# Kernel optimization log

Hardware: AMD Instinct MI355X
Metric: run time of the kernel (lower is better)

The kernel has to match this reference:

```python
import jax, jax.numpy as jnp
import numpy as np

N = 100000   # num nodes
E = 1600000  # num edges (avg degree 16)
D = 32       # input_dim == latent_size
L = 3        # num_layers
K = 3        # num_hops


def setup_inputs() -> dict:
    key = jax.random.key(0)
    k0, k1, k2, k3, k4 = jax.random.split(key, 5)
    x = jax.random.normal(k0, (N, D), dtype=jnp.float32)
    edge_index = jax.random.randint(k1, (2, E), 0, N, dtype=jnp.int32)
    edge_weight = jax.random.uniform(k2, (E,), dtype=jnp.float32)
    # TAGConv per layer: K+1 bias-free Linear(in,out) weights + one bias
    W = jax.random.normal(k3, (L, K + 1, D, D), dtype=jnp.float32) * (1.0 / np.sqrt(D))
    b = jax.random.normal(k4, (L, D), dtype=jnp.float32) * 0.01
    return {"x": x, "edge_index": edge_index, "edge_weight": edge_weight, "W": W, "b": b}


def reference(x, edge_index, edge_weight, W, b):
    row, col = edge_index[0], edge_index[1]  # source, target
    # PyG gcn_norm with add_self_loops=False: deg at target, symmetric norm
    deg = jax.ops.segment_sum(edge_weight, col, num_segments=N)
    safe = jnp.where(deg > 0, deg, 1.0)
    dis = jnp.where(deg > 0, jax.lax.rsqrt(safe), 0.0)  # deg^{-1/2}
    norm = dis[row] * edge_weight * dis[col]            # [E]
    for l in range(L):
        out = x @ W[l, 0]
        h = x
        for k in range(1, K + 1):
            # one hop of normalized sparse aggregation: out[col] += norm * h[row]
            h = jax.ops.segment_sum(h[row] * norm[:, None], col, num_segments=N)
            out = out + h @ W[l, k]
        x = jax.nn.relu(out + b[l])
    return x
```

## Files before the change

### kernel.cpp

```cpp
#include <hip/hip_runtime.h>
#include <hip/hip_fp16.h>

#define NN 100000
#define NE 1600000
#define DD 32
#define NL 3
#define NK 3

#define BK 512
#define NBK ((NN + BK - 1) / BK)
#define EA 4096
#define GA ((NE + EA - 1) / EA)
#define NCNT (NBK * GA)
#define NSC ((NCNT + 255) / 256)
#define CB (NN * DD / 4 / 256)

typedef _Float16 half8 __attribute__((ext_vector_type(8)));
typedef float f32x4 __attribute__((ext_vector_type(4)));

__global__ void countA_kernel(const int* __restrict__ col, unsigned* __restrict__ cntAB,
                              const float* __restrict__ x, __half* __restrict__ xh,
                              const float* __restrict__ W, half8* __restrict__ Bpk) {
    __shared__ unsigned hc[NBK];
    int bid = blockIdx.x;
    int t = threadIdx.x;
    if (bid < GA) {
        for (int i = t; i < NBK; i += 256) hc[i] = 0;
        __syncthreads();
        int e0 = bid * EA;
        int e1 = e0 + EA; if (e1 > NE) e1 = NE;
        for (int e = e0 + t; e < e1; e += 256)
            atomicAdd(&hc[((unsigned)col[e]) >> 9], 1u);
        __syncthreads();
        for (int i = t; i < NBK; i += 256)
            cntAB[i * GA + bid] = hc[i];
    } else if (bid < GA + CB) {
        int i = (bid - GA) * 256 + t;
        f32x4 v = ((const f32x4*)x)[i];
        __half2 h01 = __floats2half2_rn(v.x, v.y);
        __half2 h23 = __floats2half2_rn(v.z, v.w);
        int2 o;
        o.x = *(int*)&h01; o.y = *(int*)&h23;
        ((int2*)xh)[i] = o;
    } else if (t < 64) {
        int l = bid - GA - CB;
        int m = t & 15, kq = t >> 4;
        for (int c = 0; c < 4; ++c) {
            for (int h = 0; h < 2; ++h) {
                half8 hi, lo;
                for (int j = 0; j < 8; ++j) {
                    float wv = W[(size_t)((l * 4 + c) * DD + kq * 8 + j) * DD + h * 16 + m];
                    _Float16 wh = (_Float16)wv;
                    hi[j] = wh;
                    lo[j] = (_Float16)(wv - (float)wh);
                }
                Bpk[(size_t)(((l * 4 + c) * 2 + h) * 2 + 0) * 64 + t] = hi;
                Bpk[(size_t)(((l * 4 + c) * 2 + h) * 2 + 1) * 64 + t] = lo;
            }
        }
    }
}

__global__ void scanb_kernel(unsigned* __restrict__ a, unsigned* __restrict__ bsum) {
    __shared__ unsigned s[256];
    int t = threadIdx.x;
    int i = blockIdx.x * 256 + t;
    unsigned v = (i < NCNT) ? a[i] : 0u;
    s[t] = v;
    __syncthreads();
    for (int off = 1; off < 256; off <<= 1) {
        unsigned add = (t >= off) ? s[t - off] : 0u;
        __syncthreads();
        s[t] += add;
        __syncthreads();
    }
    if (i < NCNT) a[i] = s[t] - v;
    if (t == 255) bsum[blockIdx.x] = s[255];
}

__global__ void scant_kernel(unsigned* __restrict__ bsum) {
    __shared__ unsigned s[512];
    int t = threadIdx.x;
    unsigned v = (t < NSC) ? bsum[t] : 0u;
    s[t] = v;
    __syncthreads();
    for (int off = 1; off < 512; off <<= 1) {
        unsigned add = (t >= off) ? s[t - off] : 0u;
        __syncthreads();
        s[t] += add;
        __syncthreads();
    }
    if (t < NSC) bsum[t] = s[t] - v;
}

__global__ void scana_kernel(unsigned* __restrict__ a, const unsigned* __restrict__ bsum,
                             unsigned* __restrict__ bbase) {
    int i = blockIdx.x * 256 + threadIdx.x;
    if (i < NCNT) {
        unsigned v = a[i] + bsum[i >> 8];
        a[i] = v;
        if (i % GA == 0) bbase[i / GA] = v;
    }
    if (i == 0) bbase[NBK] = NE;
}

__global__ void scatterC_kernel(const int* __restrict__ row, const int* __restrict__ col,
                                const float* __restrict__ w,
                                const unsigned* __restrict__ cntAB, int2* __restrict__ eb) {
    __shared__ unsigned cur[NBK];
    int bid = blockIdx.x;
    int t = threadIdx.x;
    for (int i = t; i < NBK; i += 256) cur[i] = cntAB[i * GA + bid];
    __syncthreads();
    int e0 = bid * EA;
    int e1 = e0 + EA; if (e1 > NE) e1 = NE;
    for (int e = e0 + t; e < e1; e += 256) {
        unsigned c = (unsigned)col[e];
        unsigned pos = atomicAdd(&cur[c >> 9], 1u);
        eb[pos] = make_int2((int)(((c & 511u) << 17) | (unsigned)row[e]),
                            __float_as_int(w[e]));
    }
}

__global__ void histD1_kernel(const int2* __restrict__ eb, const unsigned* __restrict__ bbase,
                              int* __restrict__ ptr, float* __restrict__ dis) {
    __shared__ unsigned h[BK];
    __shared__ unsigned ps[256];
    int b = blockIdx.x;
    int t = threadIdx.x;
    h[t] = 0; h[t + 256] = 0;
    __syncthreads();
    unsigned e0 = bbase[b], e1 = bbase[b + 1];
    for (unsigned e = e0 + t; e < e1; e += 256) {
        int2 E = eb[e];
        unsigned cl = ((unsigned)E.x) >> 17;
        float wv = __int_as_float(E.y);
        atomicAdd(&h[cl], (1u << 24) | (unsigned)(wv * 131072.0f));
    }
    __syncthreads();
    unsigned c0 = h[2 * t] >> 24, c1 = h[2 * t + 1] >> 24;
    unsigned pv = c0 + c1;
    ps[t] = pv;
    __syncthreads();
    for (int off = 1; off < 256; off <<= 1) {
        unsigned add = (t >= off) ? ps[t - off] : 0u;
        __syncthreads();
        ps[t] += add;
        __syncthreads();
    }
    unsigned base = e0 + ps[t] - pv;
    int n0 = b * BK + 2 * t;
    if (n0 < NN) {
        ptr[n0] = (int)base;
        float dg = (float)(h[2 * t] & 0xFFFFFFu) * (1.0f / 131072.0f);
        dis[n0] = dg > 0.f ? rsqrtf(dg) : 0.f;
    }
    if (n0 + 1 < NN) {
        ptr[n0 + 1] = (int)(base + c0);
        float dg = (float)(h[2 * t + 1] & 0xFFFFFFu) * (1.0f / 131072.0f);
        dis[n0 + 1] = dg > 0.f ? rsqrtf(dg) : 0.f;
    }
    if (b == 0 && t == 0) ptr[NN] = NE;
}

__global__ void fillD2_kernel(const int2* __restrict__ eb, const unsigned* __restrict__ bbase,
                              const int* __restrict__ ptr, const float* __restrict__ dis,
                              unsigned* __restrict__ epair) {
    __shared__ unsigned cur[BK];
    __shared__ float dl[BK];
    int b = blockIdx.x;
    int t = threadIdx.x;
    int n0 = b * BK;
    for (int i = t; i < BK; i += 256) {
        int n = n0 + i;
        cur[i] = (n < NN) ? (unsigned)ptr[n] : 0u;
        dl[i] = (n < NN) ? dis[n] : 0.f;
    }
    __syncthreads();
    unsigned e0 = bbase[b], e1 = bbase[b + 1];
    for (unsigned e = e0 + t; e < e1; e += 256) {
        int2 E = eb[e];
        unsigned cl = ((unsigned)E.x) >> 17;
        unsigned r = ((unsigned)E.x) & 0x1FFFFu;
        float nv = dis[r] * __int_as_float(E.y) * dl[cl];
        unsigned pos = atomicAdd(&cur[cl], 1u);
        unsigned hb = (unsigned)__half_as_ushort(__float2half(nv));
        epair[pos] = (hb << 17) | r;
    }
}

#define ACC8(rw, vv)                                                             \
    {                                                                            \
        float2 f0 = __half22float2(*reinterpret_cast<__half2*>(&rw.x));          \
        float2 f1 = __half22float2(*reinterpret_cast<__half2*>(&rw.y));          \
        float2 f2 = __half22float2(*reinterpret_cast<__half2*>(&rw.z));          \
        float2 f3 = __half22float2(*reinterpret_cast<__half2*>(&rw.w));          \
        agg[0] = fmaf(vv, f0.x, agg[0]); agg[1] = fmaf(vv, f0.y, agg[1]);        \
        agg[2] = fmaf(vv, f1.x, agg[2]); agg[3] = fmaf(vv, f1.y, agg[3]);        \
        agg[4] = fmaf(vv, f2.x, agg[4]); agg[5] = fmaf(vv, f2.y, agg[5]);        \
        agg[6] = fmaf(vv, f3.x, agg[6]); agg[7] = fmaf(vv, f3.y, agg[7]);        \
    }

__device__ __forceinline__ void gather_body16(const ushort* __restrict__ hin,
                                              const unsigned* __restrict__ epair,
                                              int p0, int p1, int st, int c4,
                                              float agg[8]) {
    const int4* hin4 = (const int4*)hin;
    for (int e = p0 + st; e < p1; e += 16) {
        int eA = e;
        int eB = (e + 4  < p1) ? e + 4  : p1 - 1;
        int eC = (e + 8  < p1) ? e + 8  : p1 - 1;
        int eD = (e + 12 < p1) ? e + 12 : p1 - 1;
        unsigned pA = epair[eA];
        unsigned pB = epair[eB];
        unsigned pC = epair[eC];
        unsigned pD = epair[eD];
        int4 rA = hin4[(size_t)(pA & 0x1FFFFu) * 4 + c4];
        int4 rB = hin4[(size_t)(pB & 0x1FFFFu) * 4 + c4];
        int4 rC = hin4[(size_t)(pC & 0x1FFFFu) * 4 + c4];
        int4 rD = hin4[(size_t)(pD & 0x1FFFFu) * 4 + c4];
        float vA = __half2float(__ushort_as_half((unsigned short)(pA >> 17)));
        float vB = (e + 4  < p1) ? __half2float(__ushort_as_half((unsigned short)(pB >> 17))) : 0.f;
        float vC = (e + 8  < p1) ? __half2float(__ushort_as_half((unsigned short)(pC >> 17))) : 0.f;
        float vD = (e + 12 < p1) ? __half2float(__ushort_as_half((unsigned short)(pD >> 17))) : 0.f;
        ACC8(rA, vA);
        ACC8(rB, vB);
        ACC8(rC, vC);
        ACC8(rD, vD);
    }
    #pragma unroll
    for (int i = 0; i < 8; ++i) {
        agg[i] += __shfl_xor(agg[i], 4, 16);
        agg[i] += __shfl_xor(agg[i], 8, 16);
    }
}

__global__ __launch_bounds__(256) void gather_kernel(
    const ushort* __restrict__ hin, ushort* __restrict__ hout,
    const int* __restrict__ ptr, const unsigned* __restrict__ epair) {
    int tid = threadIdx.x;
    int lane16 = tid & 15;
    int st = lane16 >> 2, c4 = lane16 & 3;
    int n = blockIdx.x * 16 + (tid >> 4);
    int p0 = ptr[n], p1 = ptr[n + 1];
    float agg[8] = {0.f, 0.f, 0.f, 0.f, 0.f, 0.f, 0.f, 0.f};
    gather_body16(hin, epair, p0, p1, st, c4, agg);
    if (lane16 < 4) {
        __half2 ha = __floats2half2_rn(agg[0], agg[1]);
        __half2 hb = __floats2half2_rn(agg[2], agg[3]);
        __half2 hc = __floats2half2_rn(agg[4], agg[5]);
        __half2 hd = __floats2half2_rn(agg[6], agg[7]);
        int4 pkv;
        pkv.x = *(int*)&ha; pkv.y = *(int*)&hb;
        pkv.z = *(int*)&hc; pkv.w = *(int*)&hd;
        ((int4*)hout)[(size_t)n * 4 + lane16] = pkv;
    }
}

__global__ __launch_bounds__(256) void k3ep_kernel(
    const ushort* __restrict__ f0, const ushort* __restrict__ h1,
    const ushort* __restrict__ h2,
    ushort* __restrict__ f0out, float* __restrict__ outf,
    const int* __restrict__ ptr, const unsigned* __restrict__ epair,
    const half8* __restrict__ Bp, const float* __restrict__ bias, int last) {
    __shared__ __half ldsH[16 * DD];
    int tid = threadIdx.x;
    int lane16 = tid & 15;
    int st = lane16 >> 2, c4 = lane16 & 3;
    int nloc = tid >> 4;
    int n0 = blockIdx.x * 16;
    int n = n0 + nloc;
    int p0 = ptr[n], p1 = ptr[n + 1];
    float agg[8] = {0.f, 0.f, 0.f, 0.f, 0.f, 0.f, 0.f, 0.f};
    gather_body16(h2, epair, p0, p1, st, c4, agg);
    if (lane16 < 4) {
        __half2 ha = __floats2half2_rn(agg[0], agg[1]);
        __half2 hb = __floats2half2_rn(agg[2], agg[3]);
        __half2 hc = __floats2half2_rn(agg[4], agg[5]);
        __half2 hd = __floats2half2_rn(agg[6], agg[7]);
        int4 pkv;
        pkv.x = *(int*)&ha; pkv.y = *(int*)&hb;
        pkv.z = *(int*)&hc; pkv.w = *(int*)&hd;
        *(int4*)&ldsH[nloc * DD + lane16 * 8] = pkv;
    }
    __syncthreads();
    if (tid < 64) {
        int m = tid & 15, kq = tid >> 4;
        int ai = (n0 + m) * 4 + kq;
        const half8* A0 = (const half8*)f0;
        const half8* A1 = (const half8*)h1;
        const half8* A2 = (const half8*)h2;
        f32x4 acc0 = {0.f, 0.f, 0.f, 0.f};
        f32x4 acc1 = {0.f, 0.f, 0.f, 0.f};
        half8 a;
        a = A0[ai];
        acc0 = __builtin_amdgcn_mfma_f32_16x16x32_f16(a, Bp[0 * 64 + tid], acc0, 0, 0, 0);
        acc0 = __builtin_amdgcn_mfma_f32_16x16x32_f16(a, Bp[1 * 64 + tid], acc0, 0, 0, 0);
        acc1 = __builtin_amdgcn_mfma_f32_16x16x32_f16(a, Bp[2 * 64 + tid], acc1, 0, 0, 0);
        acc1 = __builtin_amdgcn_mfma_f32_16x16x32_f16(a, Bp[3 * 64 + tid], acc1, 0, 0, 0);
        a = A1[ai];
        acc0 = __builtin_amdgcn_mfma_f32_16x16x32_f16(a, Bp[4 * 64 + tid], acc0, 0, 0, 0);
        acc0 = __builtin_amdgcn_mfma_f32_16x16x32_f16(a, Bp[5 * 64 + tid], acc0, 0, 0, 0);
        acc1 = __builtin_amdgcn_mfma_f32_16x16x32_f16(a, Bp[6 * 64 + tid], acc1, 0, 0, 0);
        acc1 = __builtin_amdgcn_mfma_f32_16x16x32_f16(a, Bp[7 * 64 + tid], acc1, 0, 0, 0);
        a = A2[ai];
        acc0 = __builtin_amdgcn_mfma_f32_16x16x32_f16(a, Bp[8 * 64 + tid], acc0, 0, 0, 0);
        acc0 = __builtin_amdgcn_mfma_f32_16x16x32_f16(a, Bp[9 * 64 + tid], acc0, 0, 0, 0);
        acc1 = __builtin_amdgcn_mfma_f32_16x16x32_f16(a, Bp[10 * 64 + tid], acc1, 0, 0, 0);
        acc1 = __builtin_amdgcn_mfma_f32_16x16x32_f16(a, Bp[11 * 64 + tid], acc1, 0, 0, 0);
        a = *(const half8*)&ldsH[m * DD + kq * 8];
        acc0 = __builtin_amdgcn_mfma_f32_16x16x32_f16(a, Bp[12 * 64 + tid], acc0, 0, 0, 0);
        acc0 = __builtin_amdgcn_mfma_f32_16x16x32_f16(a, Bp[13 * 64 + tid], acc0, 0, 0, 0);
        acc1 = __builtin_amdgcn_mfma_f32_16x16x32_f16(a, Bp[14 * 64 + tid], acc1, 0, 0, 0);
        acc1 = __builtin_amdgcn_mfma_f32_16x16x32_f16(a, Bp[15 * 64 + tid], acc1, 0, 0, 0);
        float b0 = bias[m], b1 = bias[16 + m];
        #pragma unroll
        for (int r = 0; r < 4; ++r) {
            int rowi = n0 + kq * 4 + r;
            float v0 = fmaxf(acc0[r] + b0, 0.f);
            float v1 = fmaxf(acc1[r] + b1, 0.f);
            if (last) {
                outf[rowi * DD + m] = v0;
                outf[rowi * DD + 16 + m] = v1;
            } else {
                ((__half*)f0out)[rowi * DD + m] = __float2half(v0);
                ((__half*)f0out)[rowi * DD + 16 + m] = __float2half(v1);
            }
        }
    }
}

extern "C" void kernel_launch(void* const* d_in, const int* in_sizes, int n_in,
                              void* d_out, int out_size, void* d_ws, size_t ws_size,
                              hipStream_t stream) {
    const float* x  = (const float*)d_in[0];
    const int*   ei = (const int*)d_in[1];
    const float* ew = (const float*)d_in[2];
    const float* W  = (const float*)d_in[3];
    const float* b  = (const float*)d_in[4];
    float* out = (float*)d_out;

    const int* row = ei;
    const int* col = ei + NE;

    char* base = (char*)d_ws;
    int2*     eb    = (int2*)base;
    ushort*   h1    = (ushort*)base;
    ushort*   h2    = (ushort*)(base + 6400000);
    unsigned* epair = (unsigned*)(base + 12800000);
    ushort*   f0    = (ushort*)(base + 19200000);
    int*      ptr   = (int*)(base + 25600000);
    float*    dis   = (float*)(base + 26000016);
    unsigned* cntAB = (unsigned*)(base + 26400016);
    unsigned* bsum  = (unsigned*)(base + 26706560);
    unsigned* bbase = (unsigned*)(base + 26707776);
    half8*    Bpk   = (half8*)(base + 26708576);

    countA_kernel<<<GA + CB + NL, 256, 0, stream>>>(col, cntAB, x, (__half*)f0, W, Bpk);
    scanb_kernel<<<NSC, 256, 0, stream>>>(cntAB, bsum);
    scant_kernel<<<1, 512, 0, stream>>>(bsum);
    scana_kernel<<<NSC, 256, 0, stream>>>(cntAB, bsum, bbase);
    scatterC_kernel<<<GA, 256, 0, stream>>>(row, col, ew, cntAB, eb);
    histD1_kernel<<<NBK, 256, 0, stream>>>(eb, bbase, ptr, dis);
    fillD2_kernel<<<NBK, 256, 0, stream>>>(eb, bbase, ptr, dis, epair);

    const int grid = NN / 16;
    for (int l = 0; l < NL; ++l) {
        int lastl = (l == NL - 1);
        gather_kernel<<<grid, 256, 0, stream>>>(f0, h1, ptr, epair);
        gather_kernel<<<grid, 256, 0, stream>>>(h1, h2, ptr, epair);
        k3ep_kernel<<<grid, 256, 0, stream>>>(f0, h1, h2, f0, out, ptr, epair,
                                              Bpk + (size_t)l * 1024,
                                              b + (size_t)l * DD, lastl);
    }
}
```

Baseline: 316.9 us.

## Split each node's CSR edge list by source half for gather locality

Each destination's edge list is partitioned into sources in the lower and upper halves of the node range, with a per-node midpoint array built in the histogram pass and used in the fill pass. The gather processes the two segments one after the other, so concurrent reads of the feature table fall in one half and may hit cache more often. Edge-list loads also become nontemporal loads. The cost is extra LDS atomics and another pointer array, plus an extra loop tail per node, which adds divergence at average degree 16.

```diff
diff --git a/kernel.cpp b/kernel.cpp
--- a/kernel.cpp
+++ b/kernel.cpp
@@ -6,6 +6,7 @@
 #define DD 32
 #define NL 3
 #define NK 3
+#define NHALF (NN / 2)
 
 #define BK 512
 #define NBK ((NN + BK - 1) / BK)
@@ -123,19 +124,24 @@
 }
 
 __global__ void histD1_kernel(const int2* __restrict__ eb, const unsigned* __restrict__ bbase,
-                              int* __restrict__ ptr, float* __restrict__ dis) {
+                              int* __restrict__ ptr, int* __restrict__ ptrmid,
+                              float* __restrict__ dis) {
     __shared__ unsigned h[BK];
+    __shared__ unsigned h0[BK];
     __shared__ unsigned ps[256];
     int b = blockIdx.x;
     int t = threadIdx.x;
     h[t] = 0; h[t + 256] = 0;
+    h0[t] = 0; h0[t + 256] = 0;
     __syncthreads();
     unsigned e0 = bbase[b], e1 = bbase[b + 1];
     for (unsigned e = e0 + t; e < e1; e += 256) {
         int2 E = eb[e];
         unsigned cl = ((unsigned)E.x) >> 17;
+        unsigned r = ((unsigned)E.x) & 0x1FFFFu;
         float wv = __int_as_float(E.y);
         atomicAdd(&h[cl], (1u << 24) | (unsigned)(wv * 131072.0f));
+        if (r < (unsigned)NHALF) atomicAdd(&h0[cl], 1u);
     }
     __syncthreads();
     unsigned c0 = h[2 * t] >> 24, c1 = h[2 * t + 1] >> 24;
@@ -152,11 +158,13 @@
     int n0 = b * BK + 2 * t;
     if (n0 < NN) {
         ptr[n0] = (int)base;
+        ptrmid[n0] = (int)(base + h0[2 * t]);
         float dg = (float)(h[2 * t] & 0xFFFFFFu) * (1.0f / 131072.0f);
         dis[n0] = dg > 0.f ? rsqrtf(dg) : 0.f;
     }
     if (n0 + 1 < NN) {
         ptr[n0 + 1] = (int)(base + c0);
+        ptrmid[n0 + 1] = (int)(base + c0 + h0[2 * t + 1]);
         float dg = (float)(h[2 * t + 1] & 0xFFFFFFu) * (1.0f / 131072.0f);
         dis[n0 + 1] = dg > 0.f ? rsqrtf(dg) : 0.f;
     }
@@ -164,16 +172,18 @@
 }
 
 __global__ void fillD2_kernel(const int2* __restrict__ eb, const unsigned* __restrict__ bbase,
-                              const int* __restrict__ ptr, const float* __restrict__ dis,
-                              unsigned* __restrict__ epair) {
-    __shared__ unsigned cur[BK];
+                              const int* __restrict__ ptr, const int* __restrict__ ptrmid,
+                              const float* __restrict__ dis, unsigned* __restrict__ epair) {
+    __shared__ unsigned cur0[BK];
+    __shared__ unsigned cur1[BK];
     __shared__ float dl[BK];
     int b = blockIdx.x;
     int t = threadIdx.x;
     int n0 = b * BK;
     for (int i = t; i < BK; i += 256) {
         int n = n0 + i;
-        cur[i] = (n < NN) ? (unsigned)ptr[n] : 0u;
+        cur0[i] = (n < NN) ? (unsigned)ptr[n] : 0u;
+        cur1[i] = (n < NN) ? (unsigned)ptrmid[n] : 0u;
         dl[i] = (n < NN) ? dis[n] : 0.f;
     }
     __syncthreads();
@@ -183,7 +193,9 @@
         unsigned cl = ((unsigned)E.x) >> 17;
         unsigned r = ((unsigned)E.x) & 0x1FFFFu;
         float nv = dis[r] * __int_as_float(E.y) * dl[cl];
-        unsigned pos = atomicAdd(&cur[cl], 1u);
+        unsigned pos;
+        if (r < (unsigned)NHALF) pos = atomicAdd(&cur0[cl], 1u);
+        else                     pos = atomicAdd(&cur1[cl], 1u);
         unsigned hb = (unsigned)__half_as_ushort(__float2half(nv));
         epair[pos] = (hb << 17) | r;
     }
@@ -201,20 +213,18 @@
         agg[6] = fmaf(vv, f3.x, agg[6]); agg[7] = fmaf(vv, f3.y, agg[7]);        \
     }
 
-__device__ __forceinline__ void gather_body16(const ushort* __restrict__ hin,
-                                              const unsigned* __restrict__ epair,
-                                              int p0, int p1, int st, int c4,
-                                              float agg[8]) {
-    const int4* hin4 = (const int4*)hin;
+__device__ __forceinline__ void gather_seg(const int4* __restrict__ hin4,
+                                           const unsigned* __restrict__ epair,
+                                           int p0, int p1, int st, int c4,
+                                           float agg[8]) {
     for (int e = p0 + st; e < p1; e += 16) {
-        int eA = e;
         int eB = (e + 4  < p1) ? e + 4  : p1 - 1;
         int eC = (e + 8  < p1) ? e + 8  : p1 - 1;
         int eD = (e + 12 < p1) ? e + 12 : p1 - 1;
-        unsigned pA = epair[eA];
-        unsigned pB = epair[eB];
-        unsigned pC = epair[eC];
-        unsigned pD = epair[eD];
+        unsigned pA = __builtin_nontemporal_load(epair + e);
+        unsigned pB = __builtin_nontemporal_load(epair + eB);
+        unsigned pC = __builtin_nontemporal_load(epair + eC);
+        unsigned pD = __builtin_nontemporal_load(epair + eD);
         int4 rA = hin4[(size_t)(pA & 0x1FFFFu) * 4 + c4];
         int4 rB = hin4[(size_t)(pB & 0x1FFFFu) * 4 + c4];
         int4 rC = hin4[(size_t)(pC & 0x1FFFFu) * 4 + c4];
@@ -228,6 +238,15 @@
         ACC8(rC, vC);
         ACC8(rD, vD);
     }
+}
+
+__device__ __forceinline__ void gather_body16(const ushort* __restrict__ hin,
+                                              const unsigned* __restrict__ epair,
+                                              int p0, int pm, int p1, int st, int c4,
+                                              float agg[8]) {
+    const int4* hin4 = (const int4*)hin;
+    gather_seg(hin4, epair, p0, pm, st, c4, agg);
+    gather_seg(hin4, epair, pm, p1, st, c4, agg);
     #pragma unroll
     for (int i = 0; i < 8; ++i) {
         agg[i] += __shfl_xor(agg[i], 4, 16);
@@ -237,14 +256,15 @@
 
 __global__ __launch_bounds__(256) void gather_kernel(
     const ushort* __restrict__ hin, ushort* __restrict__ hout,
-    const int* __restrict__ ptr, const unsigned* __restrict__ epair) {
+    const int* __restrict__ ptr, const int* __restrict__ ptrmid,
+    const unsigned* __restrict__ epair) {
     int tid = threadIdx.x;
     int lane16 = tid & 15;
     int st = lane16 >> 2, c4 = lane16 & 3;
     int n = blockIdx.x * 16 + (tid >> 4);
-    int p0 = ptr[n], p1 = ptr[n + 1];
+    int p0 = ptr[n], p1 = ptr[n + 1], pm = ptrmid[n];
     float agg[8] = {0.f, 0.f, 0.f, 0.f, 0.f, 0.f, 0.f, 0.f};
-    gather_body16(hin, epair, p0, p1, st, c4, agg);
+    gather_body16(hin, epair, p0, pm, p1, st, c4, agg);
     if (lane16 < 4) {
         __half2 ha = __floats2half2_rn(agg[0], agg[1]);
         __half2 hb = __floats2half2_rn(agg[2], agg[3]);
@@ -261,7 +281,8 @@
     const ushort* __restrict__ f0, const ushort* __restrict__ h1,
     const ushort* __restrict__ h2,
     ushort* __restrict__ f0out, float* __restrict__ outf,
-    const int* __restrict__ ptr, const unsigned* __restrict__ epair,
+    const int* __restrict__ ptr, const int* __restrict__ ptrmid,
+    const unsigned* __restrict__ epair,
     const half8* __restrict__ Bp, const float* __restrict__ bias, int last) {
     __shared__ __half ldsH[16 * DD];
     int tid = threadIdx.x;
@@ -270,9 +291,9 @@
     int nloc = tid >> 4;
     int n0 = blockIdx.x * 16;
     int n = n0 + nloc;
-    int p0 = ptr[n], p1 = ptr[n + 1];
+    int p0 = ptr[n], p1 = ptr[n + 1], pm = ptrmid[n];
     float agg[8] = {0.f, 0.f, 0.f, 0.f, 0.f, 0.f, 0.f, 0.f};
-    gather_body16(h2, epair, p0, p1, st, c4, agg);
+    gather_body16(h2, epair, p0, pm, p1, st, c4, agg);
     if (lane16 < 4) {
         __half2 ha = __floats2half2_rn(agg[0], agg[1]);
         __half2 hb = __floats2half2_rn(agg[2], agg[3]);
@@ -344,32 +365,33 @@
     const int* col = ei + NE;
 
     char* base = (char*)d_ws;
-    int2*     eb    = (int2*)base;
-    ushort*   h1    = (ushort*)base;
-    ushort*   h2    = (ushort*)(base + 6400000);
-    unsigned* epair = (unsigned*)(base + 12800000);
-    ushort*   f0    = (ushort*)(base + 19200000);
-    int*      ptr   = (int*)(base + 25600000);
-    float*    dis   = (float*)(base + 26000016);
-    unsigned* cntAB = (unsigned*)(base + 26400016);
-    unsigned* bsum  = (unsigned*)(base + 26706560);
-    unsigned* bbase = (unsigned*)(base + 26707776);
-    half8*    Bpk   = (half8*)(base + 26708576);
+    int2*     eb     = (int2*)base;
+    ushort*   h1     = (ushort*)base;
+    ushort*   h2     = (ushort*)(base + 6400000);
+    unsigned* epair  = (unsigned*)(base + 12800000);
+    ushort*   f0     = (ushort*)(base + 19200000);
+    int*      ptr    = (int*)(base + 25600000);
+    float*    dis    = (float*)(base + 26000016);
+    int*      ptrmid = (int*)(base + 26400016);
+    unsigned* cntAB  = (unsigned*)(base + 26800016);
+    unsigned* bsum   = (unsigned*)(base + 27106560);
+    unsigned* bbase  = (unsigned*)(base + 27107776);
+    half8*    Bpk    = (half8*)(base + 27108576);
 
     countA_kernel<<<GA + CB + NL, 256, 0, stream>>>(col, cntAB, x, (__half*)f0, W, Bpk);
     scanb_kernel<<<NSC, 256, 0, stream>>>(cntAB, bsum);
     scant_kernel<<<1, 512, 0, stream>>>(bsum);
     scana_kernel<<<NSC, 256, 0, stream>>>(cntAB, bsum, bbase);
     scatterC_kernel<<<GA, 256, 0, stream>>>(row, col, ew, cntAB, eb);
-    histD1_kernel<<<NBK, 256, 0, stream>>>(eb, bbase, ptr, dis);
-    fillD2_kernel<<<NBK, 256, 0, stream>>>(eb, bbase, ptr, dis, epair);
+    histD1_kernel<<<NBK, 256, 0, stream>>>(eb, bbase, ptr, ptrmid, dis);
+    fillD2_kernel<<<NBK, 256, 0, stream>>>(eb, bbase, ptr, ptrmid, dis, epair);
 
     const int grid = NN / 16;
     for (int l = 0; l < NL; ++l) {
         int lastl = (l == NL - 1);
-        gather_kernel<<<grid, 256, 0, stream>>>(f0, h1, ptr, epair);
-        gather_kernel<<<grid, 256, 0, stream>>>(h1, h2, ptr, epair);
-        k3ep_kernel<<<grid, 256, 0, stream>>>(f0, h1, h2, f0, out, ptr, epair,
+        gather_kernel<<<grid, 256, 0, stream>>>(f0, h1, ptr, ptrmid, epair);
+        gather_kernel<<<grid, 256, 0, stream>>>(h1, h2, ptr, ptrmid, epair);
+        k3ep_kernel<<<grid, 256, 0, stream>>>(f0, h1, h2, f0, out, ptr, ptrmid, epair,
                                               Bpk + (size_t)l * 1024,
                                               b + (size_t)l * DD, lastl);
     }
```

Measured after the change: 353.5 us. 11.6% more time.
